# Kernel tuning notes

Hardware: AMD Instinct MI355X
Metric: run time of the kernel (lower is better)

## Reference

```python
import jax, jax.numpy as jnp
import numpy as np

B, N, F, P, E, T = 8, 10000, 8, 12, 160000, 64
C = 32  # A3TGCN2 out_channels fixed to 32 in the module


def setup_inputs() -> dict:
    key = jax.random.key(0)
    ks = jax.random.split(key, 20)
    x = jax.random.normal(ks[0], (B, N, F, P), jnp.float32)
    edge_index = jax.random.randint(ks[1], (2, E), 0, N, dtype=jnp.int64)
    edge_weight = jax.random.uniform(ks[2], (E,), jnp.float32)

    def g(k, shape):
        return jax.random.normal(k, shape, jnp.float32) * 0.05

    return dict(
        x=x, edge_index=edge_index, edge_weight=edge_weight,
        Wz=g(ks[3], (F, C)), bz=g(ks[4], (C,)),
        Wr=g(ks[5], (F, C)), br=g(ks[6], (C,)),
        Wh=g(ks[7], (F, C)), bh=g(ks[8], (C,)),
        Lz_w=g(ks[9], (2 * C, C)), Lz_b=g(ks[10], (C,)),
        Lr_w=g(ks[11], (2 * C, C)), Lr_b=g(ks[12], (C,)),
        Lh_w=g(ks[13], (2 * C, C)), Lh_b=g(ks[14], (C,)),
        att=g(ks[15], (P,)),
        lin1_w=g(ks[16], (C, P)), lin1_b=g(ks[17], (P,)),
        lin2_w=g(ks[18], (N, T)), lin2_b=g(ks[19], (T,)),
    )


def _gcn_norm(edge_index, edge_weight, n):
    # GCNConv default: add self-loops (weight 1) + symmetric normalization
    row, col = edge_index[0], edge_index[1]
    loop = jnp.arange(n)
    row = jnp.concatenate([row, loop])
    col = jnp.concatenate([col, loop])
    w = jnp.concatenate([edge_weight, jnp.ones((n,), edge_weight.dtype)])
    deg = jax.ops.segment_sum(w, col, num_segments=n)
    dis = jnp.where(deg > 0, jax.lax.rsqrt(jnp.where(deg > 0, deg, 1.0)), 0.0)
    return row, col, dis[row] * w * dis[col]


def _gcn_conv(X, W, b, row, col, norm, n):
    XW = X @ W                                   # [B,N,C]
    msg = XW[:, row, :] * norm[None, :, None]    # gather over source nodes
    out = jnp.zeros((X.shape[0], n, W.shape[1]), X.dtype).at[:, col, :].add(msg)
    return out + b


def reference(x, edge_index, edge_weight, Wz, bz, Wr, br, Wh, bh,
              Lz_w, Lz_b, Lr_w, Lr_b, Lh_w, Lh_b, att,
              lin1_w, lin1_b, lin2_w, lin2_b):
    b_, n, _, periods = x.shape
    row, col, norm = _gcn_norm(edge_index, edge_weight, n)
    probs = jax.nn.softmax(att)
    # A3TGCN2 passes H=None to the TGCN cell at every period -> hidden state
    # is zeros for every period (faithful to library implementation).
    H0 = jnp.zeros((b_, n, Lz_w.shape[1]), x.dtype)
    H_accum = jnp.zeros_like(H0)
    for p in range(periods):
        Xp = x[:, :, :, p]                       # [B,N,F]
        Z = jax.nn.sigmoid(
            jnp.concatenate([_gcn_conv(Xp, Wz, bz, row, col, norm, n), H0], axis=2) @ Lz_w + Lz_b)
        R = jax.nn.sigmoid(
            jnp.concatenate([_gcn_conv(Xp, Wr, br, row, col, norm, n), H0], axis=2) @ Lr_w + Lr_b)
        Ht = jnp.tanh(
            jnp.concatenate([_gcn_conv(Xp, Wh, bh, row, col, norm, n), H0 * R], axis=2) @ Lh_w + Lh_b)
        H = Z * H0 + (1.0 - Z) * Ht
        H_accum = H_accum + probs[p] * H
    h = jax.nn.relu(H_accum)                     # [B,N,32]
    h = h @ lin1_w + lin1_b                      # [B,N,P]
    h = jnp.swapaxes(h, 2, 1)                    # [B,P,N]
    h = h @ lin2_w + lin2_b                      # [B,P,T]
    return jnp.swapaxes(h, 2, 1)                 # [B,T,P]
```

## Files before the change

kernel.cpp:

```cpp
#include <hip/hip_runtime.h>
#include <stdint.h>

#define NN 10000
#define NNP 10016
#define NB 8
#define NP 12
#define NT 64
#define NC 32
#define BCAP 64
#define FCN 80
#define FCH 125

typedef float v2f __attribute__((ext_vector_type(2)));

__device__ __forceinline__ v2f sp(float v) { v2f r; r.x = v; r.y = v; return r; }

__global__ __launch_bounds__(1024) void k_init(
    const float* __restrict__ Wz, const float* __restrict__ bz,
    const float* __restrict__ Wh, const float* __restrict__ bh,
    const float* __restrict__ Lzw, const float* __restrict__ Lzb,
    const float* __restrict__ Lhw, const float* __restrict__ Lhb,
    const float* __restrict__ att, float* __restrict__ sm, int* __restrict__ zbase) {
    if (blockIdx.x < 20) {
        zbase[blockIdx.x * 1024 + threadIdx.x] = 0;
        return;
    }
    const int t = threadIdx.x;
    if (t >= 256) return;
    const int f = t >> 5, c = t & 31;
    float mz = 0.f, mh = 0.f;
    for (int j = 0; j < NC; ++j) {
        mz += Wz[f * NC + j] * Lzw[j * NC + c];
        mh += Wh[f * NC + j] * Lhw[j * NC + c];
    }
    sm[16 + 2 * t]     = mz;
    sm[16 + 2 * t + 1] = mh;
    if (t < NC) {
        float cz = Lzb[t], ch = Lhb[t];
        for (int j = 0; j < NC; ++j) {
            cz += bz[j] * Lzw[j * NC + t];
            ch += bh[j] * Lhw[j * NC + t];
        }
        sm[528 + 2 * t]     = cz;
        sm[528 + 2 * t + 1] = ch;
    }
    if (t == 0) {
        float m = -1e30f;
        for (int p = 0; p < NP; ++p) m = fmaxf(m, att[p]);
        float e[NP]; float s = 0.f;
        for (int p = 0; p < NP; ++p) { e[p] = __expf(att[p] - m); s += e[p]; }
        for (int p = 0; p < NP; ++p) sm[p] = e[p] / s;
    }
}

__global__ __launch_bounds__(256) void k_xform(const float* __restrict__ x,
                                               unsigned char* __restrict__ xq) {
    const int gid = blockIdx.x * 256 + threadIdx.x;
    const int s0 = gid * 2;
    const int b = s0 / 120000, rem = s0 - b * 120000;
    const int n = rem / 12, q0 = rem - n * 12;
    const int pr = b >> 1, sb = b & 1;
    const float* px = x + (size_t)b * 960000 + n * 96 + q0 * 8;
    unsigned char* pw = xq + ((size_t)(pr * NNP + n) * 192) + sb * 96 + q0 * 8;
    const float4 f0 = *(const float4*)px;
    const float4 f1 = *(const float4*)(px + 4);
    const float4 f2 = *(const float4*)(px + 8);
    const float4 f3 = *(const float4*)(px + 12);
    int u0 = __builtin_amdgcn_cvt_pk_fp8_f32(f0.x, f0.y, 0, false);
    u0     = __builtin_amdgcn_cvt_pk_fp8_f32(f0.z, f0.w, u0, true);
    int u1 = __builtin_amdgcn_cvt_pk_fp8_f32(f1.x, f1.y, 0, false);
    u1     = __builtin_amdgcn_cvt_pk_fp8_f32(f1.z, f1.w, u1, true);
    int u2 = __builtin_amdgcn_cvt_pk_fp8_f32(f2.x, f2.y, 0, false);
    u2     = __builtin_amdgcn_cvt_pk_fp8_f32(f2.z, f2.w, u2, true);
    int u3 = __builtin_amdgcn_cvt_pk_fp8_f32(f3.x, f3.y, 0, false);
    u3     = __builtin_amdgcn_cvt_pk_fp8_f32(f3.z, f3.w, u3, true);
    *(uint4*)pw = make_uint4((unsigned)u0, (unsigned)u1, (unsigned)u2, (unsigned)u3);
}

__global__ __launch_bounds__(256) void k_edge(const int* __restrict__ rowp, const int* __restrict__ colp,
                                              const float* __restrict__ ew,
                                              float* __restrict__ deg, int* __restrict__ count,
                                              uint2* __restrict__ bucket, int E) {
    const int e = blockIdx.x * 256 + threadIdx.x;
    if (e < E) {
        const int c = colp[e];
        const float w = ew[e];
        atomicAdd(&deg[c], w);
        const int slot = atomicAdd(&count[c], 1);
        if (slot < BCAP) bucket[slot * NN + c] = make_uint2((unsigned)rowp[e], __float_as_uint(w));
    }
}

#define DEC3(U0, U1, U2, ACC, W)                                                        \
    ACC[0] = __builtin_elementwise_fma((v2f)__builtin_amdgcn_cvt_pk_f32_fp8((int)(U0), false), W, ACC[0]); \
    ACC[1] = __builtin_elementwise_fma((v2f)__builtin_amdgcn_cvt_pk_f32_fp8((int)(U0), true),  W, ACC[1]); \
    ACC[2] = __builtin_elementwise_fma((v2f)__builtin_amdgcn_cvt_pk_f32_fp8((int)(U1), false), W, ACC[2]); \
    ACC[3] = __builtin_elementwise_fma((v2f)__builtin_amdgcn_cvt_pk_f32_fp8((int)(U1), true),  W, ACC[3]); \
    ACC[4] = __builtin_elementwise_fma((v2f)__builtin_amdgcn_cvt_pk_f32_fp8((int)(U2), false), W, ACC[4]); \
    ACC[5] = __builtin_elementwise_fma((v2f)__builtin_amdgcn_cvt_pk_f32_fp8((int)(U2), true),  W, ACC[5])

__global__ __launch_bounds__(64, 4) void k_main(
    const unsigned char* __restrict__ xq, const float* __restrict__ deg,
    const int* __restrict__ count, const uint2* __restrict__ bucket,
    const float* __restrict__ sm,
    const float* __restrict__ l1w, const float* __restrict__ l1b,
    float* __restrict__ h1t) {
    __shared__ float sY[16][100];
    __shared__ float sHA[16 * 33];

    const int l = threadIdx.x;
    const int pr = blockIdx.x & 3;
    const int unit = blockIdx.x >> 2;
    const int g = l >> 3, j8 = l & 7;
    const int n = unit * 8 + g;
    const char* xb = (const char*)xq + (size_t)pr * NNP * 192;
    const unsigned lo12 = (unsigned)j8 * 12u;

    const int cnt = min(count[n], BCAP);
    const float dn = rsqrtf(deg[n] + 1.0f);
    v2f A[6], B[6];
    {
        const v2f vsn = sp(dn * dn);
        const char* p0 = xb + ((unsigned)n * 192u + lo12);
        const unsigned u0 = *(const unsigned*)p0;
        const unsigned u1 = *(const unsigned*)(p0 + 4);
        const unsigned u2 = *(const unsigned*)(p0 + 8);
        const unsigned v0 = *(const unsigned*)(p0 + 96);
        const unsigned v1 = *(const unsigned*)(p0 + 100);
        const unsigned v2_ = *(const unsigned*)(p0 + 104);
        A[0] = (v2f)__builtin_amdgcn_cvt_pk_f32_fp8((int)u0, false) * vsn;
        A[1] = (v2f)__builtin_amdgcn_cvt_pk_f32_fp8((int)u0, true)  * vsn;
        A[2] = (v2f)__builtin_amdgcn_cvt_pk_f32_fp8((int)u1, false) * vsn;
        A[3] = (v2f)__builtin_amdgcn_cvt_pk_f32_fp8((int)u1, true)  * vsn;
        A[4] = (v2f)__builtin_amdgcn_cvt_pk_f32_fp8((int)u2, false) * vsn;
        A[5] = (v2f)__builtin_amdgcn_cvt_pk_f32_fp8((int)u2, true)  * vsn;
        B[0] = (v2f)__builtin_amdgcn_cvt_pk_f32_fp8((int)v0, false) * vsn;
        B[1] = (v2f)__builtin_amdgcn_cvt_pk_f32_fp8((int)v0, true)  * vsn;
        B[2] = (v2f)__builtin_amdgcn_cvt_pk_f32_fp8((int)v1, false) * vsn;
        B[3] = (v2f)__builtin_amdgcn_cvt_pk_f32_fp8((int)v1, true)  * vsn;
        B[4] = (v2f)__builtin_amdgcn_cvt_pk_f32_fp8((int)v2_, false) * vsn;
        B[5] = (v2f)__builtin_amdgcn_cvt_pk_f32_fp8((int)v2_, true)  * vsn;
    }

    int mcnt = cnt;
    #pragma unroll
    for (int off = 1; off < 64; off <<= 1) mcnt = max(mcnt, __shfl_xor(mcnt, off));

    for (int base = 0; base < mcnt; base += 8) {
        unsigned ex = 0u, ey = 0u;
        const int e = base + j8;
        if (e < cnt) {
            const uint2 be = bucket[e * NN + n];
            const float nrm = rsqrtf(deg[be.x] + 1.0f) * __uint_as_float(be.y) * dn;
            ex = be.x * 192u;
            ey = __float_as_uint(nrm);
        }
        #pragma unroll
        for (int j = 0; j < 8; ++j) {
            const int srcl = g * 8 + j;
            const unsigned e2x = (unsigned)__shfl((int)ex, srcl);
            const unsigned e2y = (unsigned)__shfl((int)ey, srcl);
            const v2f w = sp(__uint_as_float(e2y));
            const char* p = xb + (e2x + lo12);
            const unsigned u0 = *(const unsigned*)p;
            const unsigned u1 = *(const unsigned*)(p + 4);
            const unsigned u2 = *(const unsigned*)(p + 8);
            const unsigned v0 = *(const unsigned*)(p + 96);
            const unsigned v1 = *(const unsigned*)(p + 100);
            const unsigned v2_ = *(const unsigned*)(p + 104);
            DEC3(u0, u1, u2, A, w);
            DEC3(v0, v1, v2_, B, w);
        }
    }
    {
        float* ya = &sY[g * 2 + 0][j8 * 12];
        float* yb2 = &sY[g * 2 + 1][j8 * 12];
        *(float4*)ya       = make_float4(A[0].x, A[0].y, A[1].x, A[1].y);
        *(float4*)(ya + 4) = make_float4(A[2].x, A[2].y, A[3].x, A[3].y);
        *(float4*)(ya + 8) = make_float4(A[4].x, A[4].y, A[5].x, A[5].y);
        *(float4*)yb2       = make_float4(B[0].x, B[0].y, B[1].x, B[1].y);
        *(float4*)(yb2 + 4) = make_float4(B[2].x, B[2].y, B[3].x, B[3].y);
        *(float4*)(yb2 + 8) = make_float4(B[4].x, B[4].y, B[5].x, B[5].y);
    }

    const int c = l & 31;
    const float2* __restrict__ smzh = (const float2*)(sm + 16);
    const float2* __restrict__ sczh = (const float2*)(sm + 528);
    v2f m8[8];
    #pragma unroll
    for (int f = 0; f < 8; ++f) { const float2 t2 = smzh[f * 32 + c]; v2f v; v.x = t2.x; v.y = t2.y; m8[f] = v; }
    v2f czh;
    { const float2 t2 = sczh[c]; czh.x = t2.x; czh.y = t2.y; }
    float pr12[12];
    #pragma unroll
    for (int p = 0; p < 12; ++p) pr12[p] = sm[p];

    #pragma unroll
    for (int t8 = 0; t8 < 8; ++t8) {
        const int r = t8 * 2 + (l >> 5);
        const float* yb = &sY[r][0];
        v2f zh[12];
        #pragma unroll
        for (int p = 0; p < 12; ++p) zh[p] = czh;
        #pragma unroll
        for (int f = 0; f < 8; ++f) {
            const float4 y0 = *(const float4*)(yb + f * 12);
            const float4 y1 = *(const float4*)(yb + f * 12 + 4);
            const float4 y2 = *(const float4*)(yb + f * 12 + 8);
            const v2f mm = m8[f];
            zh[0]  = __builtin_elementwise_fma(sp(y0.x), mm, zh[0]);
            zh[1]  = __builtin_elementwise_fma(sp(y0.y), mm, zh[1]);
            zh[2]  = __builtin_elementwise_fma(sp(y0.z), mm, zh[2]);
            zh[3]  = __builtin_elementwise_fma(sp(y0.w), mm, zh[3]);
            zh[4]  = __builtin_elementwise_fma(sp(y1.x), mm, zh[4]);
            zh[5]  = __builtin_elementwise_fma(sp(y1.y), mm, zh[5]);
            zh[6]  = __builtin_elementwise_fma(sp(y1.z), mm, zh[6]);
            zh[7]  = __builtin_elementwise_fma(sp(y1.w), mm, zh[7]);
            zh[8]  = __builtin_elementwise_fma(sp(y2.x), mm, zh[8]);
            zh[9]  = __builtin_elementwise_fma(sp(y2.y), mm, zh[9]);
            zh[10] = __builtin_elementwise_fma(sp(y2.z), mm, zh[10]);
            zh[11] = __builtin_elementwise_fma(sp(y2.w), mm, zh[11]);
        }
        float hacc = 0.f;
        #pragma unroll
        for (int p = 0; p < 12; ++p) {
            const float u = __expf(-zh[p].x);
            const float v = __expf(2.f * zh[p].y);
            const float num = u * (v - 1.f);
            const float den = fmaf(u, v, u) + (v + 1.f);
            hacc = fmaf(pr12[p] * num, __builtin_amdgcn_rcpf(den), hacc);
        }
        sHA[r * 33 + c] = fmaxf(hacc, 0.f);
    }

    #pragma unroll
    for (int tt = 0; tt < 3; ++tt) {
        const int task = l + tt * 64;
        const int r = task / 12, p = task - r * 12;
        const int nn = unit * 8 + (r >> 1);
        if (nn < NN) {
            float s = l1b[p];
            #pragma unroll
            for (int cc = 0; cc < 32; ++cc) s = fmaf(sHA[r * 33 + cc], l1w[cc * 12 + p], s);
            h1t[nn * 96 + (pr * 2 + (r & 1)) * 12 + p] = s;
        }
    }
}

__global__ __launch_bounds__(256) void k_final(const float* __restrict__ h1t, const float* __restrict__ W2,
                                               float* __restrict__ partial) {
    __shared__ float sh1[96 * FCN];
    const int tid = threadIdx.x;
    const int n0 = blockIdx.x * FCN;

    for (int idx = tid; idx < 96 * FCN; idx += 256) {
        const int nn = idx / 96, i = idx - nn * 96;
        sh1[i * FCN + nn] = h1t[(n0 + nn) * 96 + i];
    }
    __syncthreads();

    const int t = tid & 63, w = tid >> 6;
    const float* sh = &sh1[w * 24 * FCN];
    float acc[24];
    #pragma unroll
    for (int j = 0; j < 24; ++j) acc[j] = 0.f;

    for (int nn = 0; nn < FCN; nn += 4) {
        const float w20 = W2[(n0 + nn + 0) * NT + t];
        const float w21 = W2[(n0 + nn + 1) * NT + t];
        const float w22 = W2[(n0 + nn + 2) * NT + t];
        const float w23 = W2[(n0 + nn + 3) * NT + t];
        #pragma unroll
        for (int j = 0; j < 24; ++j) {
            const float4 hv = *(const float4*)&sh[j * FCN + nn];
            acc[j] = fmaf(hv.x, w20, fmaf(hv.y, w21, fmaf(hv.z, w22, fmaf(hv.w, w23, acc[j]))));
        }
    }

    float* pp = partial + blockIdx.x * 6144 + w * 24 * 64 + t;
    #pragma unroll
    for (int j = 0; j < 24; ++j) pp[j * 64] = acc[j];
}

__global__ __launch_bounds__(256) void k_red(const float* __restrict__ partial, const float* __restrict__ l2b,
                                             float* __restrict__ out) {
    __shared__ float red[4][64];
    const int i = blockIdx.x;
    const int t = threadIdx.x & 63, g = threadIdx.x >> 6;
    float s = 0.f;
    for (int c = g; c < FCH; c += 4)
        s += partial[c * 6144 + i * 64 + t];
    red[g][t] = s;
    __syncthreads();
    if (g == 0) {
        const float v = red[0][t] + red[1][t] + red[2][t] + red[3][t] + l2b[t];
        const int b = i / 12, p = i - b * 12;
        out[b * 768 + t * 12 + p] = v;
    }
}

extern "C" void kernel_launch(void* const* d_in, const int* in_sizes, int n_in,
                              void* d_out, int out_size, void* d_ws, size_t ws_size,
                              hipStream_t stream) {
    const float* x    = (const float*)d_in[0];
    const int*   eidx = (const int*)d_in[1];
    const float* ew   = (const float*)d_in[2];
    const float* Wz   = (const float*)d_in[3];
    const float* bz   = (const float*)d_in[4];
    const float* Wh   = (const float*)d_in[7];
    const float* bh   = (const float*)d_in[8];
    const float* Lzw  = (const float*)d_in[9];
    const float* Lzb  = (const float*)d_in[10];
    const float* Lhw  = (const float*)d_in[13];
    const float* Lhb  = (const float*)d_in[14];
    const float* att  = (const float*)d_in[15];
    const float* l1w  = (const float*)d_in[16];
    const float* l1b  = (const float*)d_in[17];
    const float* W2   = (const float*)d_in[18];
    const float* l2b  = (const float*)d_in[19];
    float* out = (float*)d_out;
    const int E = in_sizes[2];
    const int EB = (E + 255) / 256;

    float* deg    = (float*)d_ws;
    int*   count  = (int*)(deg + 10240);
    uint2* bucket = (uint2*)(count + 10240);
    float* sm     = (float*)(bucket + NN * BCAP);
    float* h1t    = sm + 1024;
    unsigned char* xq = (unsigned char*)(h1t + NN * 96);
    float* partial = (float*)(xq + (size_t)4 * NNP * 192);

    const int* rowp = eidx;
    const int* colp = eidx + E;

    hipLaunchKernelGGL(k_init, dim3(21), dim3(1024), 0, stream,
                       Wz, bz, Wh, bh, Lzw, Lzb, Lhw, Lhb, att, sm, (int*)d_ws);
    hipLaunchKernelGGL(k_xform, dim3(1875), dim3(256), 0, stream, x, xq);
    hipLaunchKernelGGL(k_edge, dim3(EB), dim3(256), 0, stream, rowp, colp, ew, deg, count, bucket, E);
    hipLaunchKernelGGL(k_main, dim3(1252 * 4), dim3(64), 0, stream,
                       xq, deg, count, bucket, sm, l1w, l1b, h1t);
    hipLaunchKernelGGL(k_final, dim3(FCH), dim3(256), 0, stream, h1t, W2, partial);
    hipLaunchKernelGGL(k_red, dim3(96), dim3(256), 0, stream, partial, l2b, out);
}
```

Before: 111.6 us.

## Stage aggregated features as bf16 in LDS, use two-wave blocks, split launch

The graph-aggregated per-node features are packed to bf16 before going into shared memory and unpacked when the gate products are computed. This halves the LDS footprint and the read traffic of the staging buffer, at the cost of lower precision in an intermediate. Each block now holds two waves, each handling its own 8 nodes, instead of one wave per block. The main kernel is also split into two template launches that each cover half the nodes, which adds one kernel launch.

```diff
diff --git a/kernel.cpp b/kernel.cpp
--- a/kernel.cpp
+++ b/kernel.cpp
@@ -14,6 +14,17 @@
 typedef float v2f __attribute__((ext_vector_type(2)));
 
 __device__ __forceinline__ v2f sp(float v) { v2f r; r.x = v; r.y = v; return r; }
+__device__ __forceinline__ v2f up2(unsigned u) {
+    v2f r;
+    r.x = __uint_as_float(u << 16);
+    r.y = __uint_as_float(u & 0xffff0000u);
+    return r;
+}
+__device__ __forceinline__ unsigned pkbf(v2f a) {
+    unsigned u;
+    asm("v_cvt_pk_bf16_f32 %0, %1, %2" : "=v"(u) : "v"(a.x), "v"(a.y));
+    return u;
+}
 
 __global__ __launch_bounds__(1024) void k_init(
     const float* __restrict__ Wz, const float* __restrict__ bz,
@@ -99,20 +110,22 @@
     ACC[4] = __builtin_elementwise_fma((v2f)__builtin_amdgcn_cvt_pk_f32_fp8((int)(U2), false), W, ACC[4]); \
     ACC[5] = __builtin_elementwise_fma((v2f)__builtin_amdgcn_cvt_pk_f32_fp8((int)(U2), true),  W, ACC[5])
 
-__global__ __launch_bounds__(64, 4) void k_main(
+template<int PART>
+__global__ __launch_bounds__(128) void k_main(
     const unsigned char* __restrict__ xq, const float* __restrict__ deg,
     const int* __restrict__ count, const uint2* __restrict__ bucket,
     const float* __restrict__ sm,
     const float* __restrict__ l1w, const float* __restrict__ l1b,
     float* __restrict__ h1t) {
-    __shared__ float sY[16][100];
-    __shared__ float sHA[16 * 33];
-
-    const int l = threadIdx.x;
+    __shared__ unsigned sYb[2][16][50];
+    __shared__ float    sHA[2][528];
+
+    const int tid = threadIdx.x;
+    const int w = tid >> 6, l = tid & 63;
     const int pr = blockIdx.x & 3;
-    const int unit = blockIdx.x >> 2;
+    const int unit = PART * 313 + (blockIdx.x >> 2);
     const int g = l >> 3, j8 = l & 7;
-    const int n = unit * 8 + g;
+    const int n = unit * 16 + w * 8 + g;
     const char* xb = (const char*)xq + (size_t)pr * NNP * 192;
     const unsigned lo12 = (unsigned)j8 * 12u;
 
@@ -160,7 +173,7 @@
             const int srcl = g * 8 + j;
             const unsigned e2x = (unsigned)__shfl((int)ex, srcl);
             const unsigned e2y = (unsigned)__shfl((int)ey, srcl);
-            const v2f w = sp(__uint_as_float(e2y));
+            const v2f wq = sp(__uint_as_float(e2y));
             const char* p = xb + (e2x + lo12);
             const unsigned u0 = *(const unsigned*)p;
             const unsigned u1 = *(const unsigned*)(p + 4);
@@ -168,19 +181,17 @@
             const unsigned v0 = *(const unsigned*)(p + 96);
             const unsigned v1 = *(const unsigned*)(p + 100);
             const unsigned v2_ = *(const unsigned*)(p + 104);
-            DEC3(u0, u1, u2, A, w);
-            DEC3(v0, v1, v2_, B, w);
+            DEC3(u0, u1, u2, A, wq);
+            DEC3(v0, v1, v2_, B, wq);
         }
     }
     {
-        float* ya = &sY[g * 2 + 0][j8 * 12];
-        float* yb2 = &sY[g * 2 + 1][j8 * 12];
-        *(float4*)ya       = make_float4(A[0].x, A[0].y, A[1].x, A[1].y);
-        *(float4*)(ya + 4) = make_float4(A[2].x, A[2].y, A[3].x, A[3].y);
-        *(float4*)(ya + 8) = make_float4(A[4].x, A[4].y, A[5].x, A[5].y);
-        *(float4*)yb2       = make_float4(B[0].x, B[0].y, B[1].x, B[1].y);
-        *(float4*)(yb2 + 4) = make_float4(B[2].x, B[2].y, B[3].x, B[3].y);
-        *(float4*)(yb2 + 8) = make_float4(B[4].x, B[4].y, B[5].x, B[5].y);
+        unsigned* ya = &sYb[w][g * 2 + 0][j8 * 6];
+        unsigned* yb2 = &sYb[w][g * 2 + 1][j8 * 6];
+        ya[0] = pkbf(A[0]); ya[1] = pkbf(A[1]); ya[2] = pkbf(A[2]);
+        ya[3] = pkbf(A[3]); ya[4] = pkbf(A[4]); ya[5] = pkbf(A[5]);
+        yb2[0] = pkbf(B[0]); yb2[1] = pkbf(B[1]); yb2[2] = pkbf(B[2]);
+        yb2[3] = pkbf(B[3]); yb2[4] = pkbf(B[4]); yb2[5] = pkbf(B[5]);
     }
 
     const int c = l & 31;
@@ -198,28 +209,31 @@
     #pragma unroll
     for (int t8 = 0; t8 < 8; ++t8) {
         const int r = t8 * 2 + (l >> 5);
-        const float* yb = &sY[r][0];
+        const unsigned* yb = &sYb[w][r][0];
         v2f zh[12];
         #pragma unroll
         for (int p = 0; p < 12; ++p) zh[p] = czh;
         #pragma unroll
         for (int f = 0; f < 8; ++f) {
-            const float4 y0 = *(const float4*)(yb + f * 12);
-            const float4 y1 = *(const float4*)(yb + f * 12 + 4);
-            const float4 y2 = *(const float4*)(yb + f * 12 + 8);
+            const uint2 q0 = *(const uint2*)(yb + f * 6);
+            const uint2 q1 = *(const uint2*)(yb + f * 6 + 2);
+            const uint2 q2 = *(const uint2*)(yb + f * 6 + 4);
+            const v2f p01 = up2(q0.x), p23 = up2(q0.y);
+            const v2f p45 = up2(q1.x), p67 = up2(q1.y);
+            const v2f p89 = up2(q2.x), pAB = up2(q2.y);
             const v2f mm = m8[f];
-            zh[0]  = __builtin_elementwise_fma(sp(y0.x), mm, zh[0]);
-            zh[1]  = __builtin_elementwise_fma(sp(y0.y), mm, zh[1]);
-            zh[2]  = __builtin_elementwise_fma(sp(y0.z), mm, zh[2]);
-            zh[3]  = __builtin_elementwise_fma(sp(y0.w), mm, zh[3]);
-            zh[4]  = __builtin_elementwise_fma(sp(y1.x), mm, zh[4]);
-            zh[5]  = __builtin_elementwise_fma(sp(y1.y), mm, zh[5]);
-            zh[6]  = __builtin_elementwise_fma(sp(y1.z), mm, zh[6]);
-            zh[7]  = __builtin_elementwise_fma(sp(y1.w), mm, zh[7]);
-            zh[8]  = __builtin_elementwise_fma(sp(y2.x), mm, zh[8]);
-            zh[9]  = __builtin_elementwise_fma(sp(y2.y), mm, zh[9]);
-            zh[10] = __builtin_elementwise_fma(sp(y2.z), mm, zh[10]);
-            zh[11] = __builtin_elementwise_fma(sp(y2.w), mm, zh[11]);
+            zh[0]  = __builtin_elementwise_fma(sp(p01.x), mm, zh[0]);
+            zh[1]  = __builtin_elementwise_fma(sp(p01.y), mm, zh[1]);
+            zh[2]  = __builtin_elementwise_fma(sp(p23.x), mm, zh[2]);
+            zh[3]  = __builtin_elementwise_fma(sp(p23.y), mm, zh[3]);
+            zh[4]  = __builtin_elementwise_fma(sp(p45.x), mm, zh[4]);
+            zh[5]  = __builtin_elementwise_fma(sp(p45.y), mm, zh[5]);
+            zh[6]  = __builtin_elementwise_fma(sp(p67.x), mm, zh[6]);
+            zh[7]  = __builtin_elementwise_fma(sp(p67.y), mm, zh[7]);
+            zh[8]  = __builtin_elementwise_fma(sp(p89.x), mm, zh[8]);
+            zh[9]  = __builtin_elementwise_fma(sp(p89.y), mm, zh[9]);
+            zh[10] = __builtin_elementwise_fma(sp(pAB.x), mm, zh[10]);
+            zh[11] = __builtin_elementwise_fma(sp(pAB.y), mm, zh[11]);
         }
         float hacc = 0.f;
         #pragma unroll
@@ -230,18 +244,18 @@
             const float den = fmaf(u, v, u) + (v + 1.f);
             hacc = fmaf(pr12[p] * num, __builtin_amdgcn_rcpf(den), hacc);
         }
-        sHA[r * 33 + c] = fmaxf(hacc, 0.f);
+        sHA[w][r * 33 + c] = fmaxf(hacc, 0.f);
     }
 
     #pragma unroll
     for (int tt = 0; tt < 3; ++tt) {
         const int task = l + tt * 64;
         const int r = task / 12, p = task - r * 12;
-        const int nn = unit * 8 + (r >> 1);
+        const int nn = unit * 16 + w * 8 + (r >> 1);
         if (nn < NN) {
             float s = l1b[p];
             #pragma unroll
-            for (int cc = 0; cc < 32; ++cc) s = fmaf(sHA[r * 33 + cc], l1w[cc * 12 + p], s);
+            for (int cc = 0; cc < 32; ++cc) s = fmaf(sHA[w][r * 33 + cc], l1w[cc * 12 + p], s);
             h1t[nn * 96 + (pr * 2 + (r & 1)) * 12 + p] = s;
         }
     }
@@ -337,8 +351,8 @@
                        Wz, bz, Wh, bh, Lzw, Lzb, Lhw, Lhb, att, sm, (int*)d_ws);
     hipLaunchKernelGGL(k_xform, dim3(1875), dim3(256), 0, stream, x, xq);
     hipLaunchKernelGGL(k_edge, dim3(EB), dim3(256), 0, stream, rowp, colp, ew, deg, count, bucket, E);
-    hipLaunchKernelGGL(k_main, dim3(1252 * 4), dim3(64), 0, stream,
-                       xq, deg, count, bucket, sm, l1w, l1b, h1t);
+    k_main<0><<<dim3(313 * 4), dim3(128), 0, stream>>>(xq, deg, count, bucket, sm, l1w, l1b, h1t);
+    k_main<1><<<dim3(313 * 4), dim3(128), 0, stream>>>(xq, deg, count, bucket, sm, l1w, l1b, h1t);
     hipLaunchKernelGGL(k_final, dim3(FCH), dim3(256), 0, stream, h1t, W2, partial);
     hipLaunchKernelGGL(k_red, dim3(96), dim3(256), 0, stream, partial, l2b, out);
 }
```

Result: slower. 126.7 us (+13.5%).
